# Kernel optimization log

Measured on AMD Instinct MI355X. Metric: run time of the kernel, lower is better.

## Reference

```python
import jax, jax.numpy as jnp
import numpy as np

EPS = 1e-12  # matches torch F.normalize eps

def _l2norm(v, axis):
    n = jnp.sqrt(jnp.sum(v * v, axis=axis, keepdims=True))
    return v / jnp.maximum(n, EPS)

def setup_inputs() -> dict:
    key = jax.random.key(0)
    k1, k2, k3 = jax.random.split(key, 3)
    N, D, H, W, K = 64, 128, 56, 56, 64
    x = jax.random.normal(k1, (N, D, H, W), dtype=jnp.float32)
    conv_w = jax.random.normal(k2, (K, D), dtype=jnp.float32) * 0.05
    centroids = jax.random.uniform(k3, (K, D), dtype=jnp.float32)
    return {"x": x, "conv_w": conv_w, "centroids": centroids}

def reference(x, conv_w, centroids):
    # x: [N, D, H, W]; conv_w: [K, D] (1x1 conv, no bias); centroids: [K, D]
    N, D, H, W = x.shape
    K = centroids.shape[0]
    L = H * W
    # descriptor-wise L2 normalization over channel dim
    x = _l2norm(x, axis=1)
    xf = x.reshape(N, D, L)                      # [N, D, L]
    # 1x1 conv == per-pixel matmul; softmax over clusters
    logits = jnp.einsum('ndl,kd->nkl', xf, conv_w)  # [N, K, L]
    a = jax.nn.softmax(logits, axis=1)              # [N, K, L]
    # vlad[n,k,d] = sum_l a[n,k,l] * (x[n,d,l] - c[k,d])
    #            = (a @ x^T) - (sum_l a) * c   (matmul reformulation)
    vlad = jnp.einsum('nkl,ndl->nkd', a, xf) - a.sum(axis=-1)[:, :, None] * centroids[None]
    # intra-normalize over descriptor dim, flatten, global L2 normalize
    vlad = _l2norm(vlad, axis=2)
    vlad = vlad.reshape(N, K * D)
    vlad = _l2norm(vlad, axis=1)
    return vlad
```

## Files before the change

kernel.cpp:

```cpp
#include <hip/hip_runtime.h>
#include <hip/hip_bf16.h>

#define N_   64
#define D_   128
#define L_   3136
#define K_   64
#define TL_  64
#define NG_  8
#define ASH  72

typedef short  short8  __attribute__((ext_vector_type(8)));
typedef short  short4v __attribute__((ext_vector_type(4)));
typedef float  f32x16  __attribute__((ext_vector_type(16)));

static __device__ __forceinline__ unsigned short f2bf(float f) {
    unsigned u = __float_as_uint(f);
    return (unsigned short)((u + 0x7FFFu + ((u >> 16) & 1u)) >> 16);
}
static __device__ __forceinline__ float bf2f(short s) {
    return __uint_as_float(((unsigned)(unsigned short)s) << 16);
}
static __device__ __forceinline__ unsigned pk2(float lo, float hi) {
    __hip_bfloat162 b = __float22bfloat162_rn(make_float2(lo, hi));
    return *reinterpret_cast<unsigned*>(&b);
}

#define BARX() asm volatile("s_waitcnt lgkmcnt(0)\n\ts_barrier" ::: "memory")

#define PROCESS(VBUF, TCUR, TNEXT)                                             \
    {                                                                          \
                                    \
        _Pragma("unroll")                                                      \
        for (int j = 0; j < 4; ++j) {                                          \
            float s = 0.f;                                                     \
            _Pragma("unroll")                                                  \
            for (int r = 0; r < 8; ++r) {                                      \
                const float val = (&VBUF[r].x)[j];                             \
                s = fmaf(val, val, s);                                         \
            }                                                                  \
            red_ss[q][l0 + j] = s;                                             \
        }                                                                      \
        _Pragma("unroll")                                                      \
        for (int j = 0; j < 4; ++j) {                                          \
            const int l = l0 + j;                                              \
            union { unsigned u[4]; short8 s; } f;                              \
            f.u[0] = pk2((&VBUF[0].x)[j], (&VBUF[1].x)[j]);                    \
            f.u[1] = pk2((&VBUF[2].x)[j], (&VBUF[3].x)[j]);                    \
            f.u[2] = pk2((&VBUF[4].x)[j], (&VBUF[5].x)[j]);                    \
            f.u[3] = pk2((&VBUF[6].x)[j], (&VBUF[7].x)[j]);                    \
            *(short8*)(L1b + l * 256 + ((16 * q) ^ ((l & 15) << 4))) = f.s;    \
        }                                                                      \
        _Pragma("unroll")                                                      \
        for (int r = 0; r < 8; ++r) {                                          \
            const int d = 8 * q + r;                                           \
            union { unsigned u[2]; short4v s; } f;                             \
            f.u[0] = pk2(VBUF[r].x, VBUF[r].y);                                \
            f.u[1] = pk2(VBUF[r].z, VBUF[r].w);                                \
            *(short4v*)(L2b + d * 128 + ((l0 * 2) ^ ((d & 7) << 4))) = f.s;    \
        }                                                                      \
              \
        if ((TNEXT) < ntile) {                                                 \
            const int p0n = (tile0 + (TNEXT)) * TL_;                           \
            _Pragma("unroll")                                                  \
            for (int r = 0; r < 8; ++r)                                        \
                VBUF[r] = *(const float4*)(xb + (size_t)(8 * q + r) * L_ + p0n + l0); \
        }                                                                      \
        BARX();                                            \
        if (t < TL_) {                                                         \
            float ss = 0.f;                                                    \
            _Pragma("unroll")                                                  \
            for (int qq = 0; qq < 16; ++qq) ss += red_ss[qq][t];               \
            nrm_lds[t] = fmaxf(sqrtf(ss), 1e-12f);                             \
        }                                                                      \
                                   \
        f32x16 r1 = {0};                                                       \
        {                                                                      \
            const int l = 32 * (wv >> 1) + lm;                                 \
            const int rowoff = l * 256;                                        \
            const int swz = (l & 15) << 4;                                     \
            __builtin_amdgcn_s_setprio(1);                                     \
            _Pragma("unroll")                                                  \
            for (int ks = 0; ks < 8; ++ks) {                                   \
                const short8 bfr = *(short8*)(L1b + rowoff + (((16 * ks + 8 * lg) * 2) ^ swz)); \
                r1 = __builtin_amdgcn_mfma_f32_32x32x16_bf16(wf[ks], bfr, r1, 0, 0, 0); \
            }                                                                  \
            __builtin_amdgcn_s_setprio(0);                                     \
        }                                                                      \
        const int myl = 32 * (wv >> 1) + lm;                                   \
        float ss16 = 0.f;                                                      \
        _Pragma("unroll")                                                      \
        for (int qq = 0; qq < 16; ++qq) ss16 += red_ss[qq][myl];               \
        const float invp = 1.f / fmaxf(sqrtf(ss16), 1e-12f);                   \
                \
        float e[16];                                                           \
        float s = 0.f;                                                         \
        _Pragma("unroll")                                                      \
        for (int r = 0; r < 16; ++r) { e[r] = __expf(r1[r] * invp); s += e[r]; } \
        s += __shfl_xor(s, 32);                                                \
        if (lane < 32) dred[wv][lm] = s;                                       \
        BARX();                            \
        const float denom = dred[wv][lm] + dred[wv ^ 1][lm];                   \
        const float sc = invp / denom;                                         \
        {                                                                      \
            const int colp = 32 * (wv >> 1) + lm;                              \
            _Pragma("unroll")                                                  \
            for (int r = 0; r < 16; ++r) {                                     \
                const int k = 32 * Mt + (r & 3) + 8 * (r >> 2) + 4 * lg;       \
                AsS[k * ASH + colp] = (short)f2bf(e[r] * sc);                  \
            }                                                                  \
        }                                                                      \
        BARX();                                              \
                                \
        {                                                                      \
            short8 af[4];                                                      \
            const char* arow = AsRaw + (size_t)(32 * Mt + lm) * (ASH * 2);     \
            _Pragma("unroll")                                                  \
            for (int ks = 0; ks < 4; ++ks)                                     \
                af[ks] = *(const short8*)(arow + (16 * ks + 8 * lg) * 2);      \
            __builtin_amdgcn_s_setprio(1);                                     \
            _Pragma("unroll")                                                  \
            for (int nt = 0; nt < 2; ++nt) {                                   \
                const int dk = 32 * (2 * (wv >> 1) + nt) + lm;                 \
                const int rowoff = dk * 128;                                   \
                const int swz = (dk & 7) << 4;                                 \
                f32x16 a = (nt == 0) ? acc0 : acc1;                            \
                _Pragma("unroll")                                              \
                for (int ks = 0; ks < 4; ++ks) {                               \
                    const short8 bfr = *(short8*)(L2b + rowoff + (((16 * ks + 8 * lg) * 2) ^ swz)); \
                    a = __builtin_amdgcn_mfma_f32_32x32x16_bf16(af[ks], bfr, a, 0, 0, 0); \
                }                                                              \
                if (nt == 0) acc0 = a; else acc1 = a;                          \
            }                                                                  \
            __builtin_amdgcn_s_setprio(0);                                     \
        }                                                                      \
                                                             \
        {                                                                      \
            const int k  = 16 * wv + (lane & 15);                              \
            const int c4 = lane >> 4;                                          \
            const char* ap = AsRaw + (size_t)k * (ASH * 2) + c4 * 32;          \
            const short8 a0 = *(const short8*)ap;                              \
            const short8 a1 = *(const short8*)(ap + 16);                       \
            float ps = 0.f;                                                    \
            _Pragma("unroll")                                                  \
            for (int i = 0; i < 8; ++i) {                                      \
                ps = fmaf(bf2f(a0[i]), nrm_lds[16 * c4 + i],     ps);          \
                ps = fmaf(bf2f(a1[i]), nrm_lds[16 * c4 + 8 + i], ps);          \
            }                                                                  \
            ps += __shfl_xor(ps, 16);                                          \
            ps += __shfl_xor(ps, 32);                                          \
            asum_acc += ps;                                                    \
        }                                                                      \
        BARX();                                   \
    }

__global__ __launch_bounds__(256, 2)
void vlad_main(const float* __restrict__ x, const float* __restrict__ w,
               float* __restrict__ vout, float* __restrict__ aout,
               int vstride, int astride)
{
    __shared__ __align__(16) short L1[TL_ * D_];
    __shared__ __align__(16) short L2[D_ * TL_];
    __shared__ __align__(16) char  AsRaw[K_ * ASH * 2];
    __shared__ float nrm_lds[TL_];
    __shared__ float dred[4][32];

    const int t    = threadIdx.x;
    const int lane = t & 63;
    const int wv   = __builtin_amdgcn_readfirstlane(t >> 6);
    const int n    = blockIdx.x / NG_;
    const int g    = blockIdx.x % NG_;
    const int tile0 = (g == 0) ? 0 : (7 + 6 * (g - 1));
    const int ntile = (g == 0) ? 7 : 6;

    const int Mt = wv & 1;
    const int lg = lane >> 5;
    const int lm = lane & 31;

    char* L1b = (char*)L1;
    char* L2b = (char*)L2;
    short* AsS = (short*)AsRaw;
    float (*red_ss)[68] = (float (*)[68])AsRaw;

    short8 wf[8];
#pragma unroll
    for (int ks = 0; ks < 8; ++ks) {
        const float* wp = w + (size_t)(32 * Mt + lm) * D_ + 16 * ks + 8 * lg;
        const float4 wa = *(const float4*)wp;
        const float4 wb = *(const float4*)(wp + 4);
        union { unsigned u[4]; short8 s; } f;
        f.u[0] = pk2(wa.x, wa.y); f.u[1] = pk2(wa.z, wa.w);
        f.u[2] = pk2(wb.x, wb.y); f.u[3] = pk2(wb.z, wb.w);
        wf[ks] = f.s;
    }

    f32x16 acc0 = {0};
    f32x16 acc1 = {0};
    float asum_acc = 0.f;

    const int q  = t >> 4;
    const int l0 = (t & 15) * 4;
    const float* xb = x + (size_t)n * D_ * L_;

    float4 va[8], vb[8];
    {
        const int p0 = tile0 * TL_;
#pragma unroll
        for (int r = 0; r < 8; ++r)
            va[r] = *(const float4*)(xb + (size_t)(8 * q + r) * L_ + p0 + l0);
        const int p1 = (tile0 + 1) * TL_;
#pragma unroll
        for (int r = 0; r < 8; ++r)
            vb[r] = *(const float4*)(xb + (size_t)(8 * q + r) * L_ + p1 + l0);
    }

    for (int tp = 0; tp < ntile; tp += 2) {
        PROCESS(va, tp, tp + 2)
        if (tp + 1 < ntile) {
            PROCESS(vb, tp + 1, tp + 3)
        }
    }

    {
        const int dbase0 = 32 * (2 * (wv >> 1));
        float* vb2 = vstride ? (vout + (size_t)g * vstride) : vout;
#pragma unroll
        for (int r = 0; r < 16; ++r) {
            const int k = 32 * Mt + (r & 3) + 8 * (r >> 2) + 4 * lg;
            float* row = vb2 + ((size_t)n * K_ + k) * D_ + lm;
            if (vstride) {
                row[dbase0]      = acc0[r];
                row[dbase0 + 32] = acc1[r];
            } else {
                atomicAdd(&row[dbase0],      acc0[r]);
                atomicAdd(&row[dbase0 + 32], acc1[r]);
            }
        }
        if (lane < 16) {
            const int k = 16 * wv + lane;
            if (astride) aout[(size_t)g * astride + n * K_ + k] = asum_acc;
            else atomicAdd(&aout[n * K_ + k], asum_acc);
        }
    }
}

__global__ __launch_bounds__(256)
void vlad_fin(const float* __restrict__ vacc, const float* __restrict__ asum,
              const float* __restrict__ cent, float* __restrict__ out, int npart)
{
    const int t   = threadIdx.x;
    const int b   = blockIdx.x;
    const int n   = b >> 3;
    const int oct = b & 7;
    const int k   = oct * 8 + (t >> 5);
    const int c   = t & 31;

    float a = 0.f;
#pragma unroll 4
    for (int g = 0; g < npart; ++g) a += asum[(size_t)g * (N_ * K_) + n * K_ + k];

    const size_t off4 = ((size_t)(n * K_ + k) * D_ >> 2) + c;
    float4 v = make_float4(0.f, 0.f, 0.f, 0.f);
#pragma unroll 4
    for (int g = 0; g < npart; ++g) {
        const float4 s = ((const float4*)vacc)[(size_t)g * ((size_t)N_ * K_ * D_ >> 2) + off4];
        v.x += s.x; v.y += s.y; v.z += s.z; v.w += s.w;
    }
    const float4 cc = ((const float4*)cent)[((size_t)k * D_ >> 2) + c];
    v.x -= a * cc.x; v.y -= a * cc.y; v.z -= a * cc.z; v.w -= a * cc.w;
    float ss = v.x * v.x + v.y * v.y + v.z * v.z + v.w * v.w;
    ss += __shfl_xor(ss, 1);
    ss += __shfl_xor(ss, 2);
    ss += __shfl_xor(ss, 4);
    ss += __shfl_xor(ss, 8);
    ss += __shfl_xor(ss, 16);
    const float s1 = 0.125f / fmaxf(sqrtf(ss), 1e-12f);
    float4 o;
    o.x = v.x * s1; o.y = v.y * s1; o.z = v.z * s1; o.w = v.w * s1;
    ((float4*)out)[off4] = o;
}

extern "C" void kernel_launch(void* const* d_in, const int* in_sizes, int n_in,
                              void* d_out, int out_size, void* d_ws, size_t ws_size,
                              hipStream_t stream)
{
    const float* x = (const float*)d_in[0];
    const float* w = (const float*)d_in[1];
    const float* c = (const float*)d_in[2];
    float* out = (float*)d_out;

    const size_t vs  = (size_t)N_ * K_ * D_;
    const size_t as_ = (size_t)N_ * K_;
    const size_t need = (NG_ * vs + NG_ * as_) * sizeof(float);
    float* vacc = (float*)d_ws;

    if (ws_size >= need) {
        float* ap = vacc + NG_ * vs;
        vlad_main<<<dim3(N_ * NG_), dim3(256), 0, stream>>>(x, w, vacc, ap,
                                                            (int)vs, (int)as_);
        vlad_fin<<<dim3(N_ * 8), dim3(256), 0, stream>>>(vacc, ap, c, out, NG_);
    } else {
        float* ap = vacc + vs;
        hipMemsetAsync(d_ws, 0, (vs + as_) * sizeof(float), stream);
        vlad_main<<<dim3(N_ * NG_), dim3(256), 0, stream>>>(x, w, vacc, ap, 0, 0);
        vlad_fin<<<dim3(N_ * 8), dim3(256), 0, stream>>>(vacc, ap, c, out, 1);
    }
}
```

Measured before the change: 38.96 us.

## Double-buffer LDS tiles, drop trailing barrier, store bf16 partial VLAD slabs

The main kernel now alternates between two LDS buffers for the per-tile bf16 copies, which removes the barrier at the end of each tile. It keeps a single register prefetch set instead of two. The sum-of-squares reduction moves to wave shuffles with a smaller 4-way LDS combine, and softmax weights are packed two at a time. Partial VLAD accumulators are written to workspace as bf16 instead of fp32, halving the traffic between the two kernels at some precision cost, and the memset/atomic fallback path for small workspaces is removed.

```diff
diff --git a/kernel.cpp b/kernel.cpp
--- a/kernel.cpp
+++ b/kernel.cpp
@@ -8,15 +8,12 @@
 #define TL_  64
 #define NG_  8
 #define ASH  72
+#define VSLAB ((size_t)N_ * K_ * D_)
 
 typedef short  short8  __attribute__((ext_vector_type(8)));
 typedef short  short4v __attribute__((ext_vector_type(4)));
 typedef float  f32x16  __attribute__((ext_vector_type(16)));
 
-static __device__ __forceinline__ unsigned short f2bf(float f) {
-    unsigned u = __float_as_uint(f);
-    return (unsigned short)((u + 0x7FFFu + ((u >> 16) & 1u)) >> 16);
-}
 static __device__ __forceinline__ float bf2f(short s) {
     return __uint_as_float(((unsigned)(unsigned short)s) << 16);
 }
@@ -27,52 +24,61 @@
 
 #define BARX() asm volatile("s_waitcnt lgkmcnt(0)\n\ts_barrier" ::: "memory")
 
-#define PROCESS(VBUF, TCUR, TNEXT)                                             \
+#define PROCESS(TCUR, L1BUF, L2BUF)                                            \
     {                                                                          \
-                                    \
+        const char* L1b = (const char*)(L1BUF);                                \
+        const char* L2b = (const char*)(L2BUF);                                \
+             \
+        float s4[4];                                                           \
         _Pragma("unroll")                                                      \
         for (int j = 0; j < 4; ++j) {                                          \
             float s = 0.f;                                                     \
             _Pragma("unroll")                                                  \
             for (int r = 0; r < 8; ++r) {                                      \
-                const float val = (&VBUF[r].x)[j];                             \
+                const float val = (&v[r].x)[j];                                \
                 s = fmaf(val, val, s);                                         \
             }                                                                  \
-            red_ss[q][l0 + j] = s;                                             \
-        }                                                                      \
+            s4[j] = s;                                                         \
+        }                                                                      \
+        _Pragma("unroll")                                                      \
+        for (int j = 0; j < 4; ++j) {                                          \
+            s4[j] += __shfl_xor(s4[j], 16);                                    \
+            s4[j] += __shfl_xor(s4[j], 32);                                    \
+        }                                                                      \
+        if (lane < 16)                                                         \
+            *(float4*)&red4[wv][lane * 4] = make_float4(s4[0], s4[1], s4[2], s4[3]); \
+                           \
         _Pragma("unroll")                                                      \
         for (int j = 0; j < 4; ++j) {                                          \
             const int l = l0 + j;                                              \
             union { unsigned u[4]; short8 s; } f;                              \
-            f.u[0] = pk2((&VBUF[0].x)[j], (&VBUF[1].x)[j]);                    \
-            f.u[1] = pk2((&VBUF[2].x)[j], (&VBUF[3].x)[j]);                    \
-            f.u[2] = pk2((&VBUF[4].x)[j], (&VBUF[5].x)[j]);                    \
-            f.u[3] = pk2((&VBUF[6].x)[j], (&VBUF[7].x)[j]);                    \
-            *(short8*)(L1b + l * 256 + ((16 * q) ^ ((l & 15) << 4))) = f.s;    \
+            f.u[0] = pk2((&v[0].x)[j], (&v[1].x)[j]);                          \
+            f.u[1] = pk2((&v[2].x)[j], (&v[3].x)[j]);                          \
+            f.u[2] = pk2((&v[4].x)[j], (&v[5].x)[j]);                          \
+            f.u[3] = pk2((&v[6].x)[j], (&v[7].x)[j]);                          \
+            *(short8*)((char*)L1b + l * 256 + ((16 * q) ^ ((l & 15) << 4))) = f.s; \
         }                                                                      \
         _Pragma("unroll")                                                      \
         for (int r = 0; r < 8; ++r) {                                          \
             const int d = 8 * q + r;                                           \
             union { unsigned u[2]; short4v s; } f;                             \
-            f.u[0] = pk2(VBUF[r].x, VBUF[r].y);                                \
-            f.u[1] = pk2(VBUF[r].z, VBUF[r].w);                                \
-            *(short4v*)(L2b + d * 128 + ((l0 * 2) ^ ((d & 7) << 4))) = f.s;    \
-        }                                                                      \
-              \
-        if ((TNEXT) < ntile) {                                                 \
-            const int p0n = (tile0 + (TNEXT)) * TL_;                           \
+            f.u[0] = pk2(v[r].x, v[r].y);                                      \
+            f.u[1] = pk2(v[r].z, v[r].w);                                      \
+            *(short4v*)((char*)L2b + d * 128 + ((l0 * 2) ^ ((d & 7) << 4))) = f.s; \
+        }                                                                      \
+         \
+        if ((TCUR) + 1 < ntile) {                                              \
+            const int p0n = (tile0 + (TCUR) + 1) * TL_;                        \
             _Pragma("unroll")                                                  \
             for (int r = 0; r < 8; ++r)                                        \
-                VBUF[r] = *(const float4*)(xb + (size_t)(8 * q + r) * L_ + p0n + l0); \
-        }                                                                      \
-        BARX();                                            \
+                v[r] = *(const float4*)(xb + (size_t)(8 * q + r) * L_ + p0n + l0); \
+        }                                                                      \
+        BARX();                       \
         if (t < TL_) {                                                         \
-            float ss = 0.f;                                                    \
-            _Pragma("unroll")                                                  \
-            for (int qq = 0; qq < 16; ++qq) ss += red_ss[qq][t];               \
+            const float ss = red4[0][t] + red4[1][t] + red4[2][t] + red4[3][t]; \
             nrm_lds[t] = fmaxf(sqrtf(ss), 1e-12f);                             \
         }                                                                      \
-                                   \
+                \
         f32x16 r1 = {0};                                                       \
         {                                                                      \
             const int l = 32 * (wv >> 1) + lm;                                 \
@@ -81,15 +87,13 @@
             __builtin_amdgcn_s_setprio(1);                                     \
             _Pragma("unroll")                                                  \
             for (int ks = 0; ks < 8; ++ks) {                                   \
-                const short8 bfr = *(short8*)(L1b + rowoff + (((16 * ks + 8 * lg) * 2) ^ swz)); \
+                const short8 bfr = *(short8*)((char*)L1b + rowoff + (((16 * ks + 8 * lg) * 2) ^ swz)); \
                 r1 = __builtin_amdgcn_mfma_f32_32x32x16_bf16(wf[ks], bfr, r1, 0, 0, 0); \
             }                                                                  \
             __builtin_amdgcn_s_setprio(0);                                     \
         }                                                                      \
         const int myl = 32 * (wv >> 1) + lm;                                   \
-        float ss16 = 0.f;                                                      \
-        _Pragma("unroll")                                                      \
-        for (int qq = 0; qq < 16; ++qq) ss16 += red_ss[qq][myl];               \
+        const float ss16 = red4[0][myl] + red4[1][myl] + red4[2][myl] + red4[3][myl]; \
         const float invp = 1.f / fmaxf(sqrtf(ss16), 1e-12f);                   \
                 \
         float e[16];                                                           \
@@ -98,15 +102,18 @@
         for (int r = 0; r < 16; ++r) { e[r] = __expf(r1[r] * invp); s += e[r]; } \
         s += __shfl_xor(s, 32);                                                \
         if (lane < 32) dred[wv][lm] = s;                                       \
-        BARX();                            \
+        BARX();                             \
         const float denom = dred[wv][lm] + dred[wv ^ 1][lm];                   \
         const float sc = invp / denom;                                         \
         {                                                                      \
             const int colp = 32 * (wv >> 1) + lm;                              \
             _Pragma("unroll")                                                  \
-            for (int r = 0; r < 16; ++r) {                                     \
+            for (int rr = 0; rr < 8; ++rr) {                                   \
+                const int r = 2 * rr;                                          \
                 const int k = 32 * Mt + (r & 3) + 8 * (r >> 2) + 4 * lg;       \
-                AsS[k * ASH + colp] = (short)f2bf(e[r] * sc);                  \
+                const unsigned u = pk2(e[r] * sc, e[r + 1] * sc);              \
+                AsS[k * ASH + colp]       = (short)u;                          \
+                AsS[(k + 1) * ASH + colp] = (short)(u >> 16);                  \
             }                                                                  \
         }                                                                      \
         BARX();                                              \
@@ -126,42 +133,47 @@
                 f32x16 a = (nt == 0) ? acc0 : acc1;                            \
                 _Pragma("unroll")                                              \
                 for (int ks = 0; ks < 4; ++ks) {                               \
-                    const short8 bfr = *(short8*)(L2b + rowoff + (((16 * ks + 8 * lg) * 2) ^ swz)); \
+                    const short8 bfr = *(short8*)((char*)L2b + rowoff + (((16 * ks + 8 * lg) * 2) ^ swz)); \
                     a = __builtin_amdgcn_mfma_f32_32x32x16_bf16(af[ks], bfr, a, 0, 0, 0); \
                 }                                                              \
                 if (nt == 0) acc0 = a; else acc1 = a;                          \
             }                                                                  \
             __builtin_amdgcn_s_setprio(0);                                     \
         }                                                                      \
-                                                             \
+           \
         {                                                                      \
             const int k  = 16 * wv + (lane & 15);                              \
             const int c4 = lane >> 4;                                          \
             const char* ap = AsRaw + (size_t)k * (ASH * 2) + c4 * 32;          \
             const short8 a0 = *(const short8*)ap;                              \
             const short8 a1 = *(const short8*)(ap + 16);                       \
+            const float4* np = (const float4*)&nrm_lds[16 * c4];               \
+            const float4 n0 = np[0], n1 = np[1], n2 = np[2], n3 = np[3];       \
             float ps = 0.f;                                                    \
-            _Pragma("unroll")                                                  \
-            for (int i = 0; i < 8; ++i) {                                      \
-                ps = fmaf(bf2f(a0[i]), nrm_lds[16 * c4 + i],     ps);          \
-                ps = fmaf(bf2f(a1[i]), nrm_lds[16 * c4 + 8 + i], ps);          \
-            }                                                                  \
+            ps = fmaf(bf2f(a0[0]), n0.x, ps); ps = fmaf(bf2f(a0[1]), n0.y, ps); \
+            ps = fmaf(bf2f(a0[2]), n0.z, ps); ps = fmaf(bf2f(a0[3]), n0.w, ps); \
+            ps = fmaf(bf2f(a0[4]), n1.x, ps); ps = fmaf(bf2f(a0[5]), n1.y, ps); \
+            ps = fmaf(bf2f(a0[6]), n1.z, ps); ps = fmaf(bf2f(a0[7]), n1.w, ps); \
+            ps = fmaf(bf2f(a1[0]), n2.x, ps); ps = fmaf(bf2f(a1[1]), n2.y, ps); \
+            ps = fmaf(bf2f(a1[2]), n2.z, ps); ps = fmaf(bf2f(a1[3]), n2.w, ps); \
+            ps = fmaf(bf2f(a1[4]), n3.x, ps); ps = fmaf(bf2f(a1[5]), n3.y, ps); \
+            ps = fmaf(bf2f(a1[6]), n3.z, ps); ps = fmaf(bf2f(a1[7]), n3.w, ps); \
             ps += __shfl_xor(ps, 16);                                          \
             ps += __shfl_xor(ps, 32);                                          \
             asum_acc += ps;                                                    \
         }                                                                      \
-        BARX();                                   \
+                   \
     }
 
 __global__ __launch_bounds__(256, 2)
 void vlad_main(const float* __restrict__ x, const float* __restrict__ w,
-               float* __restrict__ vout, float* __restrict__ aout,
-               int vstride, int astride)
+               short* __restrict__ vout, float* __restrict__ aout)
 {
-    __shared__ __align__(16) short L1[TL_ * D_];
-    __shared__ __align__(16) short L2[D_ * TL_];
+    __shared__ __align__(16) short L1[2][TL_ * D_];
+    __shared__ __align__(16) short L2[2][D_ * TL_];
     __shared__ __align__(16) char  AsRaw[K_ * ASH * 2];
-    __shared__ float nrm_lds[TL_];
+    __shared__ __align__(16) float red4[4][TL_];
+    __shared__ __align__(16) float nrm_lds[TL_];
     __shared__ float dred[4][32];
 
     const int t    = threadIdx.x;
@@ -176,10 +188,7 @@
     const int lg = lane >> 5;
     const int lm = lane & 31;
 
-    char* L1b = (char*)L1;
-    char* L2b = (char*)L2;
     short* AsS = (short*)AsRaw;
-    float (*red_ss)[68] = (float (*)[68])AsRaw;
 
     short8 wf[8];
 #pragma unroll
@@ -201,51 +210,42 @@
     const int l0 = (t & 15) * 4;
     const float* xb = x + (size_t)n * D_ * L_;
 
-    float4 va[8], vb[8];
+    float4 v[8];
     {
         const int p0 = tile0 * TL_;
 #pragma unroll
         for (int r = 0; r < 8; ++r)
-            va[r] = *(const float4*)(xb + (size_t)(8 * q + r) * L_ + p0 + l0);
-        const int p1 = (tile0 + 1) * TL_;
-#pragma unroll
-        for (int r = 0; r < 8; ++r)
-            vb[r] = *(const float4*)(xb + (size_t)(8 * q + r) * L_ + p1 + l0);
+            v[r] = *(const float4*)(xb + (size_t)(8 * q + r) * L_ + p0 + l0);
     }
 
     for (int tp = 0; tp < ntile; tp += 2) {
-        PROCESS(va, tp, tp + 2)
+        PROCESS(tp, L1[0], L2[0])
         if (tp + 1 < ntile) {
-            PROCESS(vb, tp + 1, tp + 3)
+            PROCESS(tp + 1, L1[1], L2[1])
         }
     }
 
     {
         const int dbase0 = 32 * (2 * (wv >> 1));
-        float* vb2 = vstride ? (vout + (size_t)g * vstride) : vout;
+        short* vb2 = vout + (size_t)g * VSLAB;
 #pragma unroll
         for (int r = 0; r < 16; ++r) {
             const int k = 32 * Mt + (r & 3) + 8 * (r >> 2) + 4 * lg;
-            float* row = vb2 + ((size_t)n * K_ + k) * D_ + lm;
-            if (vstride) {
-                row[dbase0]      = acc0[r];
-                row[dbase0 + 32] = acc1[r];
-            } else {
-                atomicAdd(&row[dbase0],      acc0[r]);
-                atomicAdd(&row[dbase0 + 32], acc1[r]);
-            }
+            short* row = vb2 + ((size_t)n * K_ + k) * D_ + lm;
+            const unsigned u = pk2(acc0[r], acc1[r]);
+            row[dbase0]      = (short)u;
+            row[dbase0 + 32] = (short)(u >> 16);
         }
         if (lane < 16) {
             const int k = 16 * wv + lane;
-            if (astride) aout[(size_t)g * astride + n * K_ + k] = asum_acc;
-            else atomicAdd(&aout[n * K_ + k], asum_acc);
+            aout[(size_t)g * (N_ * K_) + n * K_ + k] = asum_acc;
         }
     }
 }
 
 __global__ __launch_bounds__(256)
-void vlad_fin(const float* __restrict__ vacc, const float* __restrict__ asum,
-              const float* __restrict__ cent, float* __restrict__ out, int npart)
+void vlad_fin(const short* __restrict__ vacc, const float* __restrict__ asum,
+              const float* __restrict__ cent, float* __restrict__ out)
 {
     const int t   = threadIdx.x;
     const int b   = blockIdx.x;
@@ -255,15 +255,16 @@
     const int c   = t & 31;
 
     float a = 0.f;
-#pragma unroll 4
-    for (int g = 0; g < npart; ++g) a += asum[(size_t)g * (N_ * K_) + n * K_ + k];
-
-    const size_t off4 = ((size_t)(n * K_ + k) * D_ >> 2) + c;
+#pragma unroll
+    for (int g = 0; g < NG_; ++g) a += asum[(size_t)g * (N_ * K_) + n * K_ + k];
+
+    const size_t roff = ((size_t)(n * K_ + k)) * D_ + c * 4;
     float4 v = make_float4(0.f, 0.f, 0.f, 0.f);
-#pragma unroll 4
-    for (int g = 0; g < npart; ++g) {
-        const float4 s = ((const float4*)vacc)[(size_t)g * ((size_t)N_ * K_ * D_ >> 2) + off4];
-        v.x += s.x; v.y += s.y; v.z += s.z; v.w += s.w;
+#pragma unroll
+    for (int g = 0; g < NG_; ++g) {
+        const short4v s = *(const short4v*)(vacc + (size_t)g * VSLAB + roff);
+        v.x += bf2f(s[0]); v.y += bf2f(s[1]);
+        v.z += bf2f(s[2]); v.w += bf2f(s[3]);
     }
     const float4 cc = ((const float4*)cent)[((size_t)k * D_ >> 2) + c];
     v.x -= a * cc.x; v.y -= a * cc.y; v.z -= a * cc.z; v.w -= a * cc.w;
@@ -276,7 +277,7 @@
     const float s1 = 0.125f / fmaxf(sqrtf(ss), 1e-12f);
     float4 o;
     o.x = v.x * s1; o.y = v.y * s1; o.z = v.z * s1; o.w = v.w * s1;
-    ((float4*)out)[off4] = o;
+    *(float4*)(out + roff) = o;
 }
 
 extern "C" void kernel_launch(void* const* d_in, const int* in_sizes, int n_in,
@@ -288,20 +289,9 @@
     const float* c = (const float*)d_in[2];
     float* out = (float*)d_out;
 
-    const size_t vs  = (size_t)N_ * K_ * D_;
-    const size_t as_ = (size_t)N_ * K_;
-    const size_t need = (NG_ * vs + NG_ * as_) * sizeof(float);
-    float* vacc = (float*)d_ws;
-
-    if (ws_size >= need) {
-        float* ap = vacc + NG_ * vs;
-        vlad_main<<<dim3(N_ * NG_), dim3(256), 0, stream>>>(x, w, vacc, ap,
-                                                            (int)vs, (int)as_);
-        vlad_fin<<<dim3(N_ * 8), dim3(256), 0, stream>>>(vacc, ap, c, out, NG_);
-    } else {
-        float* ap = vacc + vs;
-        hipMemsetAsync(d_ws, 0, (vs + as_) * sizeof(float), stream);
-        vlad_main<<<dim3(N_ * NG_), dim3(256), 0, stream>>>(x, w, vacc, ap, 0, 0);
-        vlad_fin<<<dim3(N_ * 8), dim3(256), 0, stream>>>(vacc, ap, c, out, 1);
-    }
-}
+    short* vacc = (short*)d_ws;
+    float* ap   = (float*)(vacc + NG_ * VSLAB);
+
+    vlad_main<<<dim3(N_ * NG_), dim3(256), 0, stream>>>(x, w, vacc, ap);
+    vlad_fin<<<dim3(N_ * 8), dim3(256), 0, stream>>>(vacc, ap, c, out);
+}
```

After: 34.41 us. 11.7% less time.
